# Performance work log

Measured on AMD Instinct MI355X. Metric: run time of the kernel, lower is better.

Reference implementation:

```python
import jax, jax.numpy as jnp
import numpy as np

N, E, F_IN, H, K = 50000, 800000, 64, 128, 4


def setup_inputs() -> dict:
    key = jax.random.key(0)
    k0, k1, k2, k3 = jax.random.split(key, 4)
    features = jax.random.normal(k0, (N, F_IN), dtype=jnp.float32)
    edge_index = jax.random.randint(k1, (2, E), 0, N, dtype=jnp.int32)
    # ChebConv parameters: one [F_IN, H] weight per Chebyshev order + shared bias
    cheb_w = jax.random.normal(k2, (K, F_IN, H), dtype=jnp.float32) * 0.05
    cheb_b = jnp.zeros((H,), dtype=jnp.float32)
    # final Linear(H, 1)
    final_w = jax.random.normal(k3, (H, 1), dtype=jnp.float32) * 0.05
    final_b = jnp.zeros((1,), dtype=jnp.float32)
    return dict(features=features, edge_index=edge_index, cheb_w=cheb_w,
                cheb_b=cheb_b, final_w=final_w, final_b=final_b)


def _cheb_conv(x, edge_index, w, b):
    # PyG ChebConv, sym normalization, lambda_max = 2.0, no self-loops in input:
    # L_hat = (2/lambda_max) * (I - D^-1/2 A D^-1/2) - I = -D^-1/2 A D^-1/2
    row, col = edge_index[0], edge_index[1]
    n = x.shape[0]
    deg = jax.ops.segment_sum(jnp.ones((row.shape[0],), dtype=x.dtype), row,
                              num_segments=n)
    dinv = jnp.where(deg > 0, jax.lax.rsqrt(jnp.maximum(deg, 1e-12)), 0.0)
    ew = -dinv[row] * dinv[col]  # [E] normalized (negated) edge weights

    def spmm(z):  # L_hat @ z via gather-multiply-scatter
        return jax.ops.segment_sum(z[col] * ew[:, None], row, num_segments=n)

    Tx0 = x
    out = Tx0 @ w[0]
    Tx1 = spmm(Tx0)
    if w.shape[0] > 1:
        out = out + Tx1 @ w[1]
    for k in range(2, w.shape[0]):  # Chebyshev recursion T_k = 2 L T_{k-1} - T_{k-2}
        Tx2 = 2.0 * spmm(Tx1) - Tx0
        out = out + Tx2 @ w[k]
        Tx0, Tx1 = Tx1, Tx2
    return out + b


def reference(features, edge_index, cheb_w, cheb_b, final_w, final_b):
    h = jnp.tanh(_cheb_conv(features, edge_index, cheb_w, cheb_b))  # [N, H]
    return (h @ final_w + final_b).reshape(-1)  # [N]
```

## Files before the change

kernel.cpp:

```cpp
#include <hip/hip_runtime.h>
#include <hip/hip_fp16.h>
#include <math.h>


#define FIN 64
#define HDIM 128

typedef _Float16 half8 __attribute__((ext_vector_type(8)));
typedef float f32x4 __attribute__((ext_vector_type(4)));

union U16 { uint4 u; __half2 h2[4]; half8 h8; };

__global__ void count_deg(const int* __restrict__ row, int* __restrict__ deg, int E) {
    int e = blockIdx.x * blockDim.x + threadIdx.x;
    if (e < E) atomicAdd(&deg[row[e]], 1);
}

__global__ void make_dinv(const int* __restrict__ deg, float* __restrict__ dinv, int n) {
    int i = blockIdx.x * blockDim.x + threadIdx.x;
    if (i < n) {
        int d = deg[i];
        dinv[i] = (d > 0) ? rsqrtf((float)d) : 0.f;
    }
}

__global__ void cvt_feat(const float4* __restrict__ src, const float* __restrict__ dinv,
                         uint4* __restrict__ dsth, uint4* __restrict__ dsts, int n8) {
    int i = blockIdx.x * blockDim.x + threadIdx.x;
    if (i >= n8) return;
    float d = dinv[i >> 3];
    float4 a = src[i * 2], b = src[i * 2 + 1];
    U16 v, vs;
    v.h2[0] = __float22half2_rn(make_float2(a.x, a.y));
    v.h2[1] = __float22half2_rn(make_float2(a.z, a.w));
    v.h2[2] = __float22half2_rn(make_float2(b.x, b.y));
    v.h2[3] = __float22half2_rn(make_float2(b.z, b.w));
    vs.h2[0] = __float22half2_rn(make_float2(d * a.x, d * a.y));
    vs.h2[1] = __float22half2_rn(make_float2(d * a.z, d * a.w));
    vs.h2[2] = __float22half2_rn(make_float2(d * b.x, d * b.y));
    vs.h2[3] = __float22half2_rn(make_float2(d * b.z, d * b.w));
    dsth[i] = v.u;
    dsts[i] = vs.u;
}

__global__ void make_bfrag(const float* __restrict__ W, uint4* __restrict__ bfrag) {
    int t = blockIdx.x * blockDim.x + threadIdx.x;
    if (t >= 8 * 8 * 64) return;
    int lane = t & 63;
    int ht = (t >> 6) & 7;
    int kk = t >> 9;
    int h = ht * 16 + (lane & 15);
    int kb = kk * 32 + (lane >> 4) * 8;
    U16 v;
#pragma unroll
    for (int j = 0; j < 4; ++j) {
        float a = W[(kb + 2 * j) * HDIM + h];
        float b = W[(kb + 2 * j + 1) * HDIM + h];
        v.h2[j] = __float22half2_rn(make_float2(a, b));
    }
    bfrag[t] = v.u;
}

__global__ void scan_local(const int* __restrict__ in, int* __restrict__ out,
                           int* __restrict__ bsum, int n) {
    __shared__ int buf[1024];
    int tid = threadIdx.x;
    int gid = blockIdx.x * 1024 + tid;
    int v = (gid < n) ? in[gid] : 0;
    int x = v;
    buf[tid] = x;
    __syncthreads();
    for (int off = 1; off < 1024; off <<= 1) {
        int t = (tid >= off) ? buf[tid - off] : 0;
        __syncthreads();
        x += t;
        buf[tid] = x;
        __syncthreads();
    }
    if (gid < n) out[gid] = x - v;
    if (tid == 1023) bsum[blockIdx.x] = x;
}

__global__ void scan_bsums(int* bsum, int nb) {
    if (blockIdx.x == 0 && threadIdx.x == 0) {
        int acc = 0;
        for (int b = 0; b < nb; ++b) { int t = bsum[b]; bsum[b] = acc; acc += t; }
    }
}

__global__ void scan_finish(int* __restrict__ rowptr, const int* __restrict__ bsum,
                            int* __restrict__ cursor, int n, int E) {
    int i = blockIdx.x * blockDim.x + threadIdx.x;
    if (i < n) {
        int v = rowptr[i] + bsum[i >> 10];
        rowptr[i] = v;
        cursor[i] = v;
    } else if (i == n) {
        rowptr[n] = E;
    }
}

__global__ void scatter_pass(const int* __restrict__ row, const int* __restrict__ col,
                             int* __restrict__ cursor, int* __restrict__ col_s,
                             int E, int r_lo, int r_hi) {
    int e = blockIdx.x * blockDim.x + threadIdx.x;
    if (e < E) {
        int r = row[e];
        if (r >= r_lo && r < r_hi) {
            int p = atomicAdd(&cursor[r], 1);
            col_s[p] = col[e];
        }
    }
}

__global__ __launch_bounds__(256) void spmm_g(
        const int* __restrict__ rowptr, const int* __restrict__ cols,
        const uint4* __restrict__ ins, const uint4* __restrict__ prevu,
        const float* __restrict__ dinv, float two,
        uint4* __restrict__ outu, uint4* __restrict__ outs, int n) {
    int lane = threadIdx.x & 63;
    int wid = (blockIdx.x * blockDim.x + threadIdx.x) >> 6;
    int li = lane & 7, g = lane >> 3;
    int r = wid * 8 + g;
    if (r >= n) return;
    int s = rowptr[r], e = rowptr[r + 1];
    float acc[8];
#pragma unroll
    for (int j = 0; j < 8; ++j) acc[j] = 0.f;
    int p = s;
    for (; p + 8 <= e; p += 8) {
        int c[8];
#pragma unroll
        for (int j = 0; j < 8; ++j) c[j] = cols[p + j];
        U16 v[8];
#pragma unroll
        for (int j = 0; j < 8; ++j) v[j].u = ins[(size_t)c[j] * 8 + li];
#pragma unroll
        for (int j = 0; j < 8; ++j) {
#pragma unroll
            for (int t = 0; t < 4; ++t) {
                float2 f = __half22float2(v[j].h2[t]);
                acc[2 * t] += f.x;
                acc[2 * t + 1] += f.y;
            }
        }
    }
    for (; p < e; ++p) {
        U16 v;
        v.u = ins[(size_t)cols[p] * 8 + li];
#pragma unroll
        for (int t = 0; t < 4; ++t) {
            float2 f = __half22float2(v.h2[t]);
            acc[2 * t] += f.x;
            acc[2 * t + 1] += f.y;
        }
    }
    float d = dinv[r];
    float rs = -d * two;
    float res[8];
    if (prevu) {
        U16 pv;
        pv.u = prevu[(size_t)r * 8 + li];
#pragma unroll
        for (int t = 0; t < 4; ++t) {
            float2 f = __half22float2(pv.h2[t]);
            res[2 * t]     = fmaf(rs, acc[2 * t], -f.x);
            res[2 * t + 1] = fmaf(rs, acc[2 * t + 1], -f.y);
        }
    } else {
#pragma unroll
        for (int j = 0; j < 8; ++j) res[j] = rs * acc[j];
    }
    U16 ru;
#pragma unroll
    for (int t = 0; t < 4; ++t)
        ru.h2[t] = __float22half2_rn(make_float2(res[2 * t], res[2 * t + 1]));
    outu[(size_t)r * 8 + li] = ru.u;
    if (outs) {
        U16 rsv;
#pragma unroll
        for (int t = 0; t < 4; ++t)
            rsv.h2[t] = __float22half2_rn(make_float2(d * res[2 * t], d * res[2 * t + 1]));
        outs[(size_t)r * 8 + li] = rsv.u;
    }
}

__device__ inline float tanh_fast(float x) {
    x = fmaxf(-10.f, fminf(10.f, x));
    float e = __expf(2.f * x);
    return (e - 1.f) / (e + 1.f);
}

__global__ __launch_bounds__(256) void gemm_mfma(
        const uint4* __restrict__ tx0, const uint4* __restrict__ tx1,
        const uint4* __restrict__ tx2, const uint4* __restrict__ tx3,
        const uint4* __restrict__ bfrag,
        const float* __restrict__ cheb_b, const float* __restrict__ fw,
        const float* __restrict__ fb, float* __restrict__ out, int n) {
    int tid = threadIdx.x;
    int lane = tid & 63;
    int wave = tid >> 6;
    int q = lane >> 4, m = lane & 15;
    int node_base = blockIdx.x * 64 + wave * 16;
    int node = node_base + m;
    size_t nd = (node < n) ? (size_t)node : 0;

    f32x4 acc[8];
#pragma unroll
    for (int t = 0; t < 8; ++t) acc[t] = (f32x4){0.f, 0.f, 0.f, 0.f};

    const uint4* txs[4] = {tx0, tx1, tx2, tx3};
#pragma unroll
    for (int kk = 0; kk < 8; ++kk) {
        U16 av;
        av.u = txs[kk >> 1][nd * 8 + (kk & 1) * 4 + q];
#pragma unroll
        for (int ht = 0; ht < 8; ++ht) {
            U16 bv;
            bv.u = bfrag[(kk * 8 + ht) * 64 + lane];
            acc[ht] = __builtin_amdgcn_mfma_f32_16x16x32_f16(av.h8, bv.h8, acc[ht], 0, 0, 0);
        }
    }

    float s[4] = {0.f, 0.f, 0.f, 0.f};
#pragma unroll
    for (int ht = 0; ht < 8; ++ht) {
        int h = ht * 16 + m;
        float cb = cheb_b[h];
        float fv = fw[h];
#pragma unroll
        for (int r = 0; r < 4; ++r)
            s[r] = fmaf(tanh_fast(acc[ht][r] + cb), fv, s[r]);
    }
#pragma unroll
    for (int r = 0; r < 4; ++r) {
        for (int msk = 1; msk < 16; msk <<= 1)
            s[r] += __shfl_xor(s[r], msk, 64);
    }
    if (m == 0) {
        float fb0 = fb[0];
#pragma unroll
        for (int r = 0; r < 4; ++r) {
            int o = node_base + q * 4 + r;
            if (o < n) out[o] = s[r] + fb0;
        }
    }
}

extern "C" void kernel_launch(void* const* d_in, const int* in_sizes, int n_in,
                              void* d_out, int out_size, void* d_ws, size_t ws_size,
                              hipStream_t stream) {
    const float* features = (const float*)d_in[0];
    const int*   edge_index = (const int*)d_in[1];
    const float* cheb_w  = (const float*)d_in[2];
    const float* cheb_b  = (const float*)d_in[3];
    const float* final_w = (const float*)d_in[4];
    const float* final_b = (const float*)d_in[5];
    int N = in_sizes[0] / FIN;
    int E = in_sizes[1] / 2;
    const int* row = edge_index;
    const int* col = edge_index + E;

    char* p = (char*)d_ws;
    auto alloc = [&](size_t bytes) {
        char* r = p;
        p += (bytes + 255) & ~(size_t)255;
        return r;
    };
    int*   deg    = (int*)alloc((size_t)N * 4);
    float* dinv   = (float*)alloc((size_t)N * 4);
    int*   rowptr = (int*)alloc((size_t)(N + 1) * 4);
    int*   cursor = (int*)alloc((size_t)N * 4);
    int*   bsum   = (int*)alloc(1024 * 4);
    int*   col_s  = (int*)alloc((size_t)E * 4);
    uint4* feath  = (uint4*)alloc((size_t)N * FIN * 2);
    uint4* feats  = (uint4*)alloc((size_t)N * FIN * 2);
    uint4* tx1h   = (uint4*)alloc((size_t)N * FIN * 2);
    uint4* tx1s   = (uint4*)alloc((size_t)N * FIN * 2);
    uint4* tx2h   = (uint4*)alloc((size_t)N * FIN * 2);
    uint4* tx2s   = (uint4*)alloc((size_t)N * FIN * 2);
    uint4* tx3h   = (uint4*)alloc((size_t)N * FIN * 2);
    uint4* bfrag  = (uint4*)alloc(4096 * 16);

    hipMemsetAsync(deg, 0, (size_t)N * 4, stream);
    count_deg<<<(E + 255) / 256, 256, 0, stream>>>(row, deg, E);
    make_dinv<<<(N + 255) / 256, 256, 0, stream>>>(deg, dinv, N);
    int n8 = N * FIN / 8;
    cvt_feat<<<(n8 + 255) / 256, 256, 0, stream>>>((const float4*)features, dinv,
                                                   feath, feats, n8);
    make_bfrag<<<16, 256, 0, stream>>>(cheb_w, bfrag);
    int nb = (N + 1023) / 1024;
    scan_local<<<nb, 1024, 0, stream>>>(deg, rowptr, bsum, N);
    scan_bsums<<<1, 64, 0, stream>>>(bsum, nb);
    scan_finish<<<(N + 1 + 255) / 256, 256, 0, stream>>>(rowptr, bsum, cursor, N, E);

    int eb = (E + 255) / 256;
    int stride = (N + 3) / 4;
    for (int pass = 0; pass < 4; ++pass) {
        int lo = pass * stride;
        int hi = (pass == 3) ? N : lo + stride;
        scatter_pass<<<eb, 256, 0, stream>>>(row, col, cursor, col_s, E, lo, hi);
    }

    int spmm_blocks = (((N + 7) / 8) * 64 + 255) / 256;
    spmm_g<<<spmm_blocks, 256, 0, stream>>>(rowptr, col_s, feats, nullptr, dinv,
                                            1.f, tx1h, tx1s, N);
    spmm_g<<<spmm_blocks, 256, 0, stream>>>(rowptr, col_s, tx1s, feath, dinv,
                                            2.f, tx2h, tx2s, N);
    spmm_g<<<spmm_blocks, 256, 0, stream>>>(rowptr, col_s, tx2s, tx1h, dinv,
                                            2.f, tx3h, nullptr, N);

    gemm_mfma<<<(N + 63) / 64, 256, 0, stream>>>(feath, tx1h, tx2h, tx3h, bfrag,
                                                 cheb_b, final_w, final_b,
                                                 (float*)d_out, N);
}
```

Measured before the change: 257.4 us.

## Map one wavefront per row in SpMM with cross-group shuffle reduction

The SpMM kernel now assigns a full 64-lane wavefront to each row instead of 8 rows per wavefront. The eight 8-lane groups each handle a different neighbor in parallel, and partial sums are combined with xor shuffles before one group writes the result. The aim is more memory-level parallelism per row and less tail imbalance from the sequential per-row neighbor loop. The cost is eight times more waves, shuffle reduction overhead, and idle lanes on low-degree rows (average degree is about 16).

```diff
diff --git a/kernel.cpp b/kernel.cpp
--- a/kernel.cpp
+++ b/kernel.cpp
@@ -113,75 +113,92 @@
     }
 }
 
-__global__ __launch_bounds__(256) void spmm_g(
+__global__ __launch_bounds__(256) void spmm_row(
         const int* __restrict__ rowptr, const int* __restrict__ cols,
         const uint4* __restrict__ ins, const uint4* __restrict__ prevu,
         const float* __restrict__ dinv, float two,
         uint4* __restrict__ outu, uint4* __restrict__ outs, int n) {
     int lane = threadIdx.x & 63;
-    int wid = (blockIdx.x * blockDim.x + threadIdx.x) >> 6;
-    int li = lane & 7, g = lane >> 3;
-    int r = wid * 8 + g;
+    int r = (blockIdx.x * blockDim.x + threadIdx.x) >> 6;
     if (r >= n) return;
+    int g = lane >> 3, li = lane & 7;
     int s = rowptr[r], e = rowptr[r + 1];
     float acc[8];
 #pragma unroll
     for (int j = 0; j < 8; ++j) acc[j] = 0.f;
+
     int p = s;
+    for (; p + 16 <= e; p += 16) {
+        int c0 = cols[p + g];
+        int c1 = cols[p + 8 + g];
+        U16 v0, v1;
+        v0.u = ins[(size_t)c0 * 8 + li];
+        v1.u = ins[(size_t)c1 * 8 + li];
+#pragma unroll
+        for (int t = 0; t < 4; ++t) {
+            float2 f0 = __half22float2(v0.h2[t]);
+            float2 f1 = __half22float2(v1.h2[t]);
+            acc[2 * t]     += f0.x + f1.x;
+            acc[2 * t + 1] += f0.y + f1.y;
+        }
+    }
     for (; p + 8 <= e; p += 8) {
-        int c[8];
-#pragma unroll
-        for (int j = 0; j < 8; ++j) c[j] = cols[p + j];
-        U16 v[8];
-#pragma unroll
-        for (int j = 0; j < 8; ++j) v[j].u = ins[(size_t)c[j] * 8 + li];
-#pragma unroll
-        for (int j = 0; j < 8; ++j) {
+        int c0 = cols[p + g];
+        U16 v0;
+        v0.u = ins[(size_t)c0 * 8 + li];
+#pragma unroll
+        for (int t = 0; t < 4; ++t) {
+            float2 f0 = __half22float2(v0.h2[t]);
+            acc[2 * t]     += f0.x;
+            acc[2 * t + 1] += f0.y;
+        }
+    }
+    if (p + g < e) {
+        int c0 = cols[p + g];
+        U16 v0;
+        v0.u = ins[(size_t)c0 * 8 + li];
+#pragma unroll
+        for (int t = 0; t < 4; ++t) {
+            float2 f0 = __half22float2(v0.h2[t]);
+            acc[2 * t]     += f0.x;
+            acc[2 * t + 1] += f0.y;
+        }
+    }
+#pragma unroll
+    for (int j = 0; j < 8; ++j) {
+        acc[j] += __shfl_xor(acc[j], 8, 64);
+        acc[j] += __shfl_xor(acc[j], 16, 64);
+        acc[j] += __shfl_xor(acc[j], 32, 64);
+    }
+    if (g == 0) {
+        float d = dinv[r];
+        float rs = -d * two;
+        float res[8];
+        if (prevu) {
+            U16 pv;
+            pv.u = prevu[(size_t)r * 8 + li];
 #pragma unroll
             for (int t = 0; t < 4; ++t) {
-                float2 f = __half22float2(v[j].h2[t]);
-                acc[2 * t] += f.x;
-                acc[2 * t + 1] += f.y;
+                float2 f = __half22float2(pv.h2[t]);
+                res[2 * t]     = fmaf(rs, acc[2 * t], -f.x);
+                res[2 * t + 1] = fmaf(rs, acc[2 * t + 1], -f.y);
             }
-        }
-    }
-    for (; p < e; ++p) {
-        U16 v;
-        v.u = ins[(size_t)cols[p] * 8 + li];
-#pragma unroll
-        for (int t = 0; t < 4; ++t) {
-            float2 f = __half22float2(v.h2[t]);
-            acc[2 * t] += f.x;
-            acc[2 * t + 1] += f.y;
-        }
-    }
-    float d = dinv[r];
-    float rs = -d * two;
-    float res[8];
-    if (prevu) {
-        U16 pv;
-        pv.u = prevu[(size_t)r * 8 + li];
-#pragma unroll
-        for (int t = 0; t < 4; ++t) {
-            float2 f = __half22float2(pv.h2[t]);
-            res[2 * t]     = fmaf(rs, acc[2 * t], -f.x);
-            res[2 * t + 1] = fmaf(rs, acc[2 * t + 1], -f.y);
-        }
-    } else {
-#pragma unroll
-        for (int j = 0; j < 8; ++j) res[j] = rs * acc[j];
-    }
-    U16 ru;
-#pragma unroll
-    for (int t = 0; t < 4; ++t)
-        ru.h2[t] = __float22half2_rn(make_float2(res[2 * t], res[2 * t + 1]));
-    outu[(size_t)r * 8 + li] = ru.u;
-    if (outs) {
-        U16 rsv;
+        } else {
+#pragma unroll
+            for (int j = 0; j < 8; ++j) res[j] = rs * acc[j];
+        }
+        U16 ru;
 #pragma unroll
         for (int t = 0; t < 4; ++t)
-            rsv.h2[t] = __float22half2_rn(make_float2(d * res[2 * t], d * res[2 * t + 1]));
-        outs[(size_t)r * 8 + li] = rsv.u;
+            ru.h2[t] = __float22half2_rn(make_float2(res[2 * t], res[2 * t + 1]));
+        outu[(size_t)r * 8 + li] = ru.u;
+        if (outs) {
+            U16 rsv;
+#pragma unroll
+            for (int t = 0; t < 4; ++t)
+                rsv.h2[t] = __float22half2_rn(make_float2(d * res[2 * t], d * res[2 * t + 1]));
+            outs[(size_t)r * 8 + li] = rsv.u;
+        }
     }
 }
 
@@ -302,13 +319,13 @@
         scatter_pass<<<eb, 256, 0, stream>>>(row, col, cursor, col_s, E, lo, hi);
     }
 
-    int spmm_blocks = (((N + 7) / 8) * 64 + 255) / 256;
-    spmm_g<<<spmm_blocks, 256, 0, stream>>>(rowptr, col_s, feats, nullptr, dinv,
-                                            1.f, tx1h, tx1s, N);
-    spmm_g<<<spmm_blocks, 256, 0, stream>>>(rowptr, col_s, tx1s, feath, dinv,
-                                            2.f, tx2h, tx2s, N);
-    spmm_g<<<spmm_blocks, 256, 0, stream>>>(rowptr, col_s, tx2s, tx1h, dinv,
-                                            2.f, tx3h, nullptr, N);
+    int spmm_blocks = ((size_t)N * 64 + 255) / 256;
+    spmm_row<<<spmm_blocks, 256, 0, stream>>>(rowptr, col_s, feats, nullptr, dinv,
+                                              1.f, tx1h, tx1s, N);
+    spmm_row<<<spmm_blocks, 256, 0, stream>>>(rowptr, col_s, tx1s, feath, dinv,
+                                              2.f, tx2h, tx2s, N);
+    spmm_row<<<spmm_blocks, 256, 0, stream>>>(rowptr, col_s, tx2s, tx1h, dinv,
+                                              2.f, tx3h, nullptr, N);
 
     gemm_mfma<<<(N + 63) / 64, 256, 0, stream>>>(feath, tx1h, tx2h, tx3h, bfrag,
                                                  cheb_b, final_w, final_b,
```

After: 267.9 us. +4.1%, slower.
